# Performance work log

Measured on AMD Instinct MI355X. Metric: run time of the kernel, lower is better.

Reference implementation:

```python
import math
import jax, jax.numpy as jnp
import numpy as np

CH = 256
NUM_GROUPS = 32
EPS = 1e-5


def setup_inputs() -> dict:
    key = jax.random.key(0)
    ks = jax.random.split(key, 8)
    B, C, S = 32, CH, 32
    x = jax.random.normal(ks[0], (B, C, S, S), dtype=jnp.float32)
    t_embd = jax.random.normal(ks[1], (B, 4 * C), dtype=jnp.float32)
    gamma = jnp.ones((C,), dtype=jnp.float32)
    beta = jnp.zeros((C,), dtype=jnp.float32)
    # torch nn.Linear(ch, 3*ch): weight shape (3*ch, ch), y = x @ W.T + b
    w_attn = jax.random.normal(ks[2], (3 * C, C), dtype=jnp.float32) * (1.0 / math.sqrt(C))
    b_attn = jax.random.normal(ks[3], (3 * C,), dtype=jnp.float32) * 0.02
    w_proj = jax.random.normal(ks[4], (C, C), dtype=jnp.float32) * (1.0 / math.sqrt(C))
    b_proj = jax.random.normal(ks[5], (C,), dtype=jnp.float32) * 0.02
    return {
        "x": x, "t_embd": t_embd,
        "gamma": gamma, "beta": beta,
        "w_attn": w_attn, "b_attn": b_attn,
        "w_proj": w_proj, "b_proj": b_proj,
    }


def _group_norm(x, gamma, beta):
    # x: (B, C, S, S), normalize over (C/G, S, S) per group
    B, C, S, _ = x.shape
    xg = x.reshape(B, NUM_GROUPS, (C // NUM_GROUPS) * S * S)
    mean = jnp.mean(xg, axis=-1, keepdims=True)
    var = jnp.var(xg, axis=-1, keepdims=True)
    xn = ((xg - mean) * jax.lax.rsqrt(var + EPS)).reshape(B, C, S, S)
    return xn * gamma[None, :, None, None] + beta[None, :, None, None]


def reference(x, t_embd, gamma, beta, w_attn, b_attn, w_proj, b_proj):
    B, C, S, _ = x.shape
    norm_x = _group_norm(x, gamma, beta)
    h = jnp.transpose(norm_x, (0, 2, 3, 1))            # (B, S, S, C)
    qkv = h @ w_attn.T + b_attn                        # (B, S, S, 3C)
    q, k, v = jnp.split(qkv, 3, axis=3)
    # full spatial attention: scores over all S*S key positions
    att = jnp.einsum('bhwc,bHWc->bhwHW', q, k) * (1.0 / math.sqrt(C))
    att = jax.nn.softmax(att.reshape(B, S, S, S * S), axis=-1).reshape(B, S, S, S, S)
    o = jnp.einsum('bhwHW,bHWc->bhwc', att, v)         # (B, S, S, C)
    y = o @ w_proj.T + b_proj
    y = jnp.transpose(y, (0, 3, 1, 2))                 # (B, C, S, S)
    return x + y
```

## Files before the change

### kernel.cpp

```cpp
#include <hip/hip_runtime.h>
#include <hip/hip_bf16.h>
#include <stdint.h>
#include <stddef.h>


typedef float  f32x4  __attribute__((ext_vector_type(4)));
typedef __bf16 bf16x8 __attribute__((ext_vector_type(8)));
typedef __bf16 bf16x4 __attribute__((ext_vector_type(4)));

#define DEVI static __device__ __forceinline__

DEVI f32x4 mfma16(bf16x8 a, bf16x8 b, f32x4 c) {
  return __builtin_amdgcn_mfma_f32_16x16x32_bf16(a, b, c, 0, 0, 0);
}

DEVI f32x4 zero4() { f32x4 z = {0.f, 0.f, 0.f, 0.f}; return z; }

typedef const __attribute__((address_space(1))) void* gas_cvp;
typedef __attribute__((address_space(3))) void*       las_vp;

DEVI void gl_lds16(const __bf16* g, __bf16* l) {
  __builtin_amdgcn_global_load_lds((gas_cvp)g, (las_vp)l, 16, 0, 0);
}

#define WAIT_VM(N) asm volatile("s_waitcnt vmcnt(" #N ")" ::: "memory")
DEVI void bar() {
  asm volatile("" ::: "memory");
  __builtin_amdgcn_s_barrier();
  asm volatile("" ::: "memory");
}

__global__ __launch_bounds__(256) void cvt_weights(
    const float* __restrict__ wa, const float* __restrict__ wp,
    __bf16* __restrict__ wab, __bf16* __restrict__ wpb) {
  const int i = blockIdx.x * 256 + threadIdx.x;
  if (i < 196608) {
    wab[i] = (__bf16)wa[i];
  } else {
    const int j = i - 196608;
    if (j < 65536) wpb[j] = (__bf16)wp[j];
  }
}

__global__ __launch_bounds__(256) void gn_fused(
    const float* __restrict__ x, const float* __restrict__ gamma,
    const float* __restrict__ beta, __bf16* __restrict__ h) {
  __shared__ __align__(16) float xs[8192];
  __shared__ float redS[4], redSS[4];
  const int bg = blockIdx.x;
  const int b = bg >> 5, g = bg & 31;
  const int tid = threadIdx.x;
  const float* base = x + (size_t)bg * 8192;
  float s = 0.f, ss = 0.f;
#pragma unroll
  for (int it = 0; it < 8; ++it) {
    const int i = it * 256 + tid;
    f32x4 v = *(const f32x4*)(base + i * 4);
    *(f32x4*)(xs + i * 4) = v;
    s  += v[0] + v[1] + v[2] + v[3];
    ss += v[0]*v[0] + v[1]*v[1] + v[2]*v[2] + v[3]*v[3];
  }
#pragma unroll
  for (int m = 1; m < 64; m <<= 1) {
    s  += __shfl_xor(s,  m, 64);
    ss += __shfl_xor(ss, m, 64);
  }
  const int lane = tid & 63, wave = tid >> 6;
  if (lane == 0) { redS[wave] = s; redSS[wave] = ss; }
  __syncthreads();
  const float S  = redS[0] + redS[1] + redS[2] + redS[3];
  const float SS = redSS[0] + redSS[1] + redSS[2] + redSS[3];
  const float mu = S * (1.f / 8192.f);
  const float rstd = rsqrtf(SS * (1.f / 8192.f) - mu * mu + 1e-5f);
  float ga[8], be[8];
#pragma unroll
  for (int j = 0; j < 8; ++j) {
    const int c = g * 8 + j;
    ga[j] = gamma[c] * rstd;
    be[j] = beta[c] - mu * ga[j];
  }
  __bf16* hb = h + ((size_t)b << 18) + g * 8;
#pragma unroll
  for (int it = 0; it < 4; ++it) {
    const int p = it * 256 + tid;
    bf16x8 o8;
#pragma unroll
    for (int j = 0; j < 8; ++j)
      o8[j] = (__bf16)(xs[j * 1024 + p] * ga[j] + be[j]);
    *(bf16x8*)(hb + ((size_t)p << 8)) = o8;
  }
}

DEVI void gemm_core_k256(const __bf16* __restrict__ A0, const __bf16* __restrict__ B0,
                         __bf16* lA, __bf16* lB, int lane, int wave, f32x4 acc[4][4]) {
  const int wm = (wave >> 1) * 64;
  const int wn = (wave & 1) * 64;
  const int r15 = lane & 15, lg = lane >> 4;
#pragma unroll
  for (int i = 0; i < 4; ++i)
#pragma unroll
    for (int j = 0; j < 4; ++j) acc[i][j] = zero4();

  for (int ko = 0; ko < 4; ++ko) {
#pragma unroll
    for (int it = 0; it < 4; ++it) {
      const int q = wave * 256 + it * 64 + lane;
      const int row = q >> 3, c8 = q & 7;
      const int srcoff = row * 256 + ko * 64 + ((c8 ^ (row & 7)) << 3);
      gl_lds16(A0 + srcoff, lA + (size_t)(wave * 256 + it * 64) * 8);
      gl_lds16(B0 + srcoff, lB + (size_t)(wave * 256 + it * 64) * 8);
    }
    __syncthreads();
#pragma unroll
    for (int kk = 0; kk < 2; ++kk) {
      bf16x8 af[4], bfr[4];
#pragma unroll
      for (int i = 0; i < 4; ++i) {
        const int row = wm + i * 16 + r15;
        af[i] = *(const bf16x8*)((const char*)lA + row * 128 +
                                 (((kk * 4 + lg) ^ (row & 7)) << 4));
      }
#pragma unroll
      for (int j = 0; j < 4; ++j) {
        const int row = wn + j * 16 + r15;
        bfr[j] = *(const bf16x8*)((const char*)lB + row * 128 +
                                  (((kk * 4 + lg) ^ (row & 7)) << 4));
      }
#pragma unroll
      for (int i = 0; i < 4; ++i)
#pragma unroll
        for (int j = 0; j < 4; ++j) acc[i][j] = mfma16(af[i], bfr[j], acc[i][j]);
    }
    __syncthreads();
  }
}

__global__ __launch_bounds__(256) void qkv_gemm(
    const __bf16* __restrict__ h, const __bf16* __restrict__ wab,
    const float* __restrict__ b_attn,
    __bf16* __restrict__ q, __bf16* __restrict__ k, __bf16* __restrict__ vt) {
  __shared__ __align__(16) __bf16 lA[128 * 64], lB[128 * 64];
  const int nt = blockIdx.x, mt = blockIdx.y;
  const int tid = threadIdx.x, lane = tid & 63, wave = tid >> 6;
  f32x4 acc[4][4];
  gemm_core_k256(h + (size_t)mt * 128 * 256, wab + (size_t)nt * 128 * 256,
                 lA, lB, lane, wave, acc);

  const int wm = (wave >> 1) * 64, wn = (wave & 1) * 64;
  const int r15 = lane & 15, lg = lane >> 4;
  const int sec = nt >> 1;
  const float QS = 0.0625f * 1.44269504088896340736f;
#pragma unroll
  for (int j = 0; j < 4; ++j) {
    const int ng = nt * 128 + wn + j * 16 + r15;
    const float bias = b_attn[ng];
    const int c = ng & 255;
#pragma unroll
    for (int i = 0; i < 4; ++i) {
      const int mbase = mt * 128 + wm + i * 16 + lg * 4;
      if (sec == 0) {
#pragma unroll
        for (int r = 0; r < 4; ++r)
          q[(size_t)(mbase + r) * 256 + c] = (__bf16)((acc[i][j][r] + bias) * QS);
      } else if (sec == 1) {
#pragma unroll
        for (int r = 0; r < 4; ++r)
          k[(size_t)(mbase + r) * 256 + c] = (__bf16)(acc[i][j][r] + bias);
      } else {
        const int b = mbase >> 10, p = mbase & 1023;
        bf16x4 pk;
#pragma unroll
        for (int r = 0; r < 4; ++r) pk[r] = (__bf16)(acc[i][j][r] + bias);
        *(bf16x4*)(vt + (((size_t)(b * 256 + c)) << 10) + p) = pk;
      }
    }
  }
}

__global__ __launch_bounds__(512, 2) void attn(
    const __bf16* __restrict__ q, const __bf16* __restrict__ k,
    const __bf16* __restrict__ vt, __bf16* __restrict__ o) {
  extern __shared__ __align__(16) char smem[];

  const int bid = blockIdx.x;
  const int xcd = bid & 7, sub = bid >> 3;
  const int b = xcd * 4 + (sub & 3);
  const int qt = sub >> 2;
  const int tid = threadIdx.x, lane = tid & 63, wave = tid >> 6;
  const int r15 = lane & 15, lg = lane >> 4, rs7 = r15 & 7;
  const int m0 = qt * 128 + wave * 16;
  char* P = smem + 131072 + wave * 2048;

  const __bf16* kb = k  + ((size_t)b << 18);
  const __bf16* vb = vt + ((size_t)b << 18);

  const __bf16* qb = q + (((size_t)(b * 1024 + m0)) << 8);
  bf16x8 qf[8];
#pragma unroll
  for (int kc = 0; kc < 8; ++kc)
    qf[kc] = *(const bf16x8*)(qb + ((size_t)r15) * 256 + kc * 32 + lg * 8);

  f32x4 po[16];
#pragma unroll
  for (int d = 0; d < 16; ++d) po[d] = zero4();
  float mrun = -1e30f, lrun = 0.f;

  auto stageK = [&](int n0, int buf) {
    __bf16* dst = (__bf16*)(smem + buf * 32768);
#pragma unroll
    for (int it = 0; it < 4; ++it) {
      const int qch = it * 512 + tid;
      const int row = qch >> 5, c32 = qch & 31;
      gl_lds16(kb + (size_t)(n0 + row) * 256 + ((c32 ^ (row & 7)) << 3),
               dst + (size_t)(it * 512 + wave * 64) * 8);
    }
  };
  auto stageV = [&](int n0, int buf) {
    __bf16* dst = (__bf16*)(smem + 65536 + buf * 32768);
#pragma unroll
    for (int it = 0; it < 4; ++it) {
      const int qch = it * 512 + tid;
      const int row = qch >> 3, c8 = qch & 7;
      gl_lds16(vb + ((size_t)row << 10) + n0 + ((c8 ^ (row & 7)) << 3),
               dst + (size_t)(it * 512 + wave * 64) * 8);
    }
  };

  stageK(0, 0);
  stageV(0, 0);

  for (int kv = 0; kv < 16; ++kv) {
    const int cur = kv & 1;
    const char* lK = (const char*)smem + cur * 32768;
    const char* lV = (const char*)smem + 65536 + cur * 32768;
    if (kv < 15) {
      stageK((kv + 1) * 64, cur ^ 1);
      stageV((kv + 1) * 64, cur ^ 1);
      WAIT_VM(8);
    } else {
      WAIT_VM(0);
    }
    bar();

    f32x4 s[4];
#pragma unroll
    for (int j = 0; j < 4; ++j) s[j] = zero4();
#pragma unroll
    for (int kc = 0; kc < 8; ++kc) {
      bf16x8 kf[4];
#pragma unroll
      for (int j = 0; j < 4; ++j)
        kf[j] = *(const bf16x8*)(lK + (j * 16 + r15) * 512 +
                                 (((kc * 4 + lg) ^ rs7) << 4));
#pragma unroll
      for (int j = 0; j < 4; ++j) s[j] = mfma16(kf[j], qf[kc], s[j]);
    }
    float pmax = s[0][0];
#pragma unroll
    for (int j = 0; j < 4; ++j)
#pragma unroll
      for (int r = 0; r < 4; ++r) pmax = fmaxf(pmax, s[j][r]);
    pmax = fmaxf(pmax, __shfl_xor(pmax, 16, 64));
    pmax = fmaxf(pmax, __shfl_xor(pmax, 32, 64));
    if (!__all(pmax <= mrun + 8.f)) {
      const float mn = fmaxf(mrun, pmax);
      const float scl = exp2f(mrun - mn);
      mrun = mn;
      lrun *= scl;
#pragma unroll
      for (int d = 0; d < 16; ++d) po[d] *= scl;
    }
    float psum = 0.f;
    bf16x4 pk[4];
#pragma unroll
    for (int j = 0; j < 4; ++j)
#pragma unroll
      for (int r = 0; r < 4; ++r) {
        const float pv = exp2f(s[j][r] - mrun);
        psum += pv;
        pk[j][r] = (__bf16)pv;
      }
    psum += __shfl_xor(psum, 16, 64);
    psum += __shfl_xor(psum, 32, 64);
    lrun += psum;
#pragma unroll
    for (int j = 0; j < 4; ++j)
      *(bf16x4*)(P + r15 * 128 + ((j * 32 + lg * 8) ^ (rs7 << 4))) = pk[j];
#pragma unroll
    for (int kk = 0; kk < 2; ++kk) {
      const bf16x8 pb =
          *(const bf16x8*)(P + r15 * 128 + (((kk * 4 + lg) ^ rs7) << 4));
#pragma unroll
      for (int df = 0; df < 16; ++df) {
        const bf16x8 vf = *(const bf16x8*)(lV + (df * 16 + r15) * 128 +
                                           (((kk * 4 + lg) ^ rs7) << 4));
        po[df] = mfma16(vf, pb, po[df]);
      }
    }
    bar();
  }
  const float inv = 1.f / lrun;
  __bf16* ob = o + (((size_t)(b * 1024 + m0 + r15)) << 8);
#pragma unroll
  for (int df = 0; df < 16; ++df) {
    bf16x4 t;
#pragma unroll
    for (int r = 0; r < 4; ++r) t[r] = (__bf16)(po[df][r] * inv);
    *(bf16x4*)(ob + df * 16 + lg * 4) = t;
  }
}

__global__ __launch_bounds__(256) void proj_gemm(
    const __bf16* __restrict__ o, const __bf16* __restrict__ wpb,
    const float* __restrict__ b_proj, const float* __restrict__ x,
    float* __restrict__ out) {
  __shared__ __align__(16) __bf16 lA[128 * 64], lB[128 * 64];
  const int nt = blockIdx.x, mt = blockIdx.y;
  const int tid = threadIdx.x, lane = tid & 63, wave = tid >> 6;
  f32x4 acc[4][4];
  gemm_core_k256(o + (size_t)mt * 128 * 256, wpb + (size_t)nt * 128 * 256,
                 lA, lB, lane, wave, acc);

  const int wm = (wave >> 1) * 64, wn = (wave & 1) * 64;
  const int r15 = lane & 15, lg = lane >> 4;
#pragma unroll
  for (int j = 0; j < 4; ++j) {
    const int c = nt * 128 + wn + j * 16 + r15;
    const float bias = b_proj[c];
#pragma unroll
    for (int i = 0; i < 4; ++i) {
      const int mbase = mt * 128 + wm + i * 16 + lg * 4;
      const int b = mbase >> 10, p = mbase & 1023;
      const size_t off = (((size_t)(b * 256 + c)) << 10) + p;
      f32x4 xv = *(const f32x4*)(x + off);
      f32x4 r = acc[i][j];
      r = r + xv;
      r = r + bias;
      *(f32x4*)(out + off) = r;
    }
  }
}

extern "C" void kernel_launch(void* const* d_in, const int* in_sizes, int n_in,
                              void* d_out, int out_size, void* d_ws, size_t ws_size,
                              hipStream_t stream) {
  const float* x      = (const float*)d_in[0];
  const float* gamma  = (const float*)d_in[2];
  const float* beta   = (const float*)d_in[3];
  const float* w_attn = (const float*)d_in[4];
  const float* b_attn = (const float*)d_in[5];
  const float* w_proj = (const float*)d_in[6];
  const float* b_proj = (const float*)d_in[7];
  float* out = (float*)d_out;

  char* ws = (char*)d_ws;
  __bf16* h   = (__bf16*)(ws);
  __bf16* qb  = (__bf16*)(ws + ((size_t)16 << 20));
  __bf16* kb  = (__bf16*)(ws + ((size_t)32 << 20));
  __bf16* vtb = (__bf16*)(ws + ((size_t)48 << 20));
  __bf16* wab = (__bf16*)(ws + ((size_t)64 << 20));
  __bf16* wpb = wab + 196608;

  cvt_weights<<<1024, 256, 0, stream>>>(w_attn, w_proj, wab, wpb);
  gn_fused<<<1024, 256, 0, stream>>>(x, gamma, beta, h);
  qkv_gemm<<<dim3(6, 256), 256, 0, stream>>>(h, wab, b_attn, qb, kb, vtb);
  attn<<<256, 512, 147456, stream>>>(qb, kb, vtb, h );
  proj_gemm<<<dim3(2, 256), 256, 0, stream>>>(h, wpb, b_proj, x, out);
}
```

Baseline: 131.6 us.

## Double query rows per attention wave and load full K in GEMMs

The attention kernel now runs 4 waves per block, each handling 32 query rows as two 16-row halves. This lets every K and V fragment read from LDS feed two MFMAs, halving LDS traffic per FLOP at the cost of doubled accumulator registers. The QKV and projection GEMMs now stage the whole K=256 slice into 128KB of dynamic LDS in one pass, removing the per-k-chunk barriers. The trade-off is occupancy of one block per CU and no overlap of load with compute.

```diff
diff --git a/kernel.cpp b/kernel.cpp
--- a/kernel.cpp
+++ b/kernel.cpp
@@ -91,8 +91,8 @@
   }
 }
 
-DEVI void gemm_core_k256(const __bf16* __restrict__ A0, const __bf16* __restrict__ B0,
-                         __bf16* lA, __bf16* lB, int lane, int wave, f32x4 acc[4][4]) {
+DEVI void gemm_full(const __bf16* __restrict__ A0, const __bf16* __restrict__ B0,
+                    __bf16* lA, __bf16* lB, int lane, int wave, f32x4 acc[4][4]) {
   const int wm = (wave >> 1) * 64;
   const int wn = (wave & 1) * 64;
   const int r15 = lane & 15, lg = lane >> 4;
@@ -101,50 +101,49 @@
 #pragma unroll
     for (int j = 0; j < 4; ++j) acc[i][j] = zero4();
 
-  for (int ko = 0; ko < 4; ++ko) {
-#pragma unroll
-    for (int it = 0; it < 4; ++it) {
-      const int q = wave * 256 + it * 64 + lane;
-      const int row = q >> 3, c8 = q & 7;
-      const int srcoff = row * 256 + ko * 64 + ((c8 ^ (row & 7)) << 3);
-      gl_lds16(A0 + srcoff, lA + (size_t)(wave * 256 + it * 64) * 8);
-      gl_lds16(B0 + srcoff, lB + (size_t)(wave * 256 + it * 64) * 8);
-    }
-    __syncthreads();
-#pragma unroll
-    for (int kk = 0; kk < 2; ++kk) {
-      bf16x8 af[4], bfr[4];
-#pragma unroll
-      for (int i = 0; i < 4; ++i) {
-        const int row = wm + i * 16 + r15;
-        af[i] = *(const bf16x8*)((const char*)lA + row * 128 +
-                                 (((kk * 4 + lg) ^ (row & 7)) << 4));
-      }
-#pragma unroll
-      for (int j = 0; j < 4; ++j) {
-        const int row = wn + j * 16 + r15;
-        bfr[j] = *(const bf16x8*)((const char*)lB + row * 128 +
-                                  (((kk * 4 + lg) ^ (row & 7)) << 4));
-      }
-#pragma unroll
-      for (int i = 0; i < 4; ++i)
-#pragma unroll
-        for (int j = 0; j < 4; ++j) acc[i][j] = mfma16(af[i], bfr[j], acc[i][j]);
-    }
-    __syncthreads();
-  }
-}
-
-__global__ __launch_bounds__(256) void qkv_gemm(
+#pragma unroll
+  for (int it = 0; it < 16; ++it) {
+    const int qch = it * 256 + wave * 64 + lane;
+    const int row = qch >> 5, c32 = qch & 31;
+    const int src = row * 256 + ((c32 ^ (row & 7)) << 3);
+    gl_lds16(A0 + src, lA + (size_t)(it * 256 + wave * 64) * 8);
+    gl_lds16(B0 + src, lB + (size_t)(it * 256 + wave * 64) * 8);
+  }
+  __syncthreads();
+#pragma unroll
+  for (int kk = 0; kk < 8; ++kk) {
+    bf16x8 af[4], bfr[4];
+#pragma unroll
+    for (int i = 0; i < 4; ++i) {
+      const int row = wm + i * 16 + r15;
+      af[i] = *(const bf16x8*)((const char*)lA + row * 512 +
+                               (((kk * 4 + lg) ^ (row & 7)) << 4));
+    }
+#pragma unroll
+    for (int j = 0; j < 4; ++j) {
+      const int row = wn + j * 16 + r15;
+      bfr[j] = *(const bf16x8*)((const char*)lB + row * 512 +
+                                (((kk * 4 + lg) ^ (row & 7)) << 4));
+    }
+#pragma unroll
+    for (int i = 0; i < 4; ++i)
+#pragma unroll
+      for (int j = 0; j < 4; ++j) acc[i][j] = mfma16(af[i], bfr[j], acc[i][j]);
+  }
+}
+
+__global__ __launch_bounds__(256, 1) void qkv_gemm(
     const __bf16* __restrict__ h, const __bf16* __restrict__ wab,
     const float* __restrict__ b_attn,
     __bf16* __restrict__ q, __bf16* __restrict__ k, __bf16* __restrict__ vt) {
-  __shared__ __align__(16) __bf16 lA[128 * 64], lB[128 * 64];
+  extern __shared__ __align__(16) char gsm[];
+  __bf16* lA = (__bf16*)gsm;
+  __bf16* lB = (__bf16*)(gsm + 65536);
   const int nt = blockIdx.x, mt = blockIdx.y;
   const int tid = threadIdx.x, lane = tid & 63, wave = tid >> 6;
   f32x4 acc[4][4];
-  gemm_core_k256(h + (size_t)mt * 128 * 256, wab + (size_t)nt * 128 * 256,
-                 lA, lB, lane, wave, acc);
+  gemm_full(h + (size_t)mt * 128 * 256, wab + (size_t)nt * 128 * 256,
+            lA, lB, lane, wave, acc);
 
   const int wm = (wave >> 1) * 64, wn = (wave & 1) * 64;
   const int r15 = lane & 15, lg = lane >> 4;
@@ -177,7 +176,7 @@
   }
 }
 
-__global__ __launch_bounds__(512, 2) void attn(
+__global__ __launch_bounds__(256, 1) void attn(
     const __bf16* __restrict__ q, const __bf16* __restrict__ k,
     const __bf16* __restrict__ vt, __bf16* __restrict__ o) {
   extern __shared__ __align__(16) char smem[];
@@ -188,41 +187,45 @@
   const int qt = sub >> 2;
   const int tid = threadIdx.x, lane = tid & 63, wave = tid >> 6;
   const int r15 = lane & 15, lg = lane >> 4, rs7 = r15 & 7;
-  const int m0 = qt * 128 + wave * 16;
-  char* P = smem + 131072 + wave * 2048;
+  const int m0 = qt * 128 + wave * 32;
+  char* P = smem + 131072 + wave * 4096;
 
   const __bf16* kb = k  + ((size_t)b << 18);
   const __bf16* vb = vt + ((size_t)b << 18);
 
   const __bf16* qb = q + (((size_t)(b * 1024 + m0)) << 8);
-  bf16x8 qf[8];
-#pragma unroll
-  for (int kc = 0; kc < 8; ++kc)
-    qf[kc] = *(const bf16x8*)(qb + ((size_t)r15) * 256 + kc * 32 + lg * 8);
-
-  f32x4 po[16];
-#pragma unroll
-  for (int d = 0; d < 16; ++d) po[d] = zero4();
-  float mrun = -1e30f, lrun = 0.f;
+  bf16x8 qf[2][8];
+#pragma unroll
+  for (int qh = 0; qh < 2; ++qh)
+#pragma unroll
+    for (int kc = 0; kc < 8; ++kc)
+      qf[qh][kc] = *(const bf16x8*)(qb + (size_t)(qh * 16 + r15) * 256 + kc * 32 + lg * 8);
+
+  f32x4 po[16][2];
+#pragma unroll
+  for (int d = 0; d < 16; ++d)
+#pragma unroll
+    for (int qh = 0; qh < 2; ++qh) po[d][qh] = zero4();
+  float mrun[2] = {-1e30f, -1e30f}, lrun[2] = {0.f, 0.f};
 
   auto stageK = [&](int n0, int buf) {
     __bf16* dst = (__bf16*)(smem + buf * 32768);
 #pragma unroll
-    for (int it = 0; it < 4; ++it) {
-      const int qch = it * 512 + tid;
+    for (int it = 0; it < 8; ++it) {
+      const int qch = it * 256 + tid;
       const int row = qch >> 5, c32 = qch & 31;
       gl_lds16(kb + (size_t)(n0 + row) * 256 + ((c32 ^ (row & 7)) << 3),
-               dst + (size_t)(it * 512 + wave * 64) * 8);
+               dst + (size_t)(it * 256 + wave * 64) * 8);
     }
   };
   auto stageV = [&](int n0, int buf) {
     __bf16* dst = (__bf16*)(smem + 65536 + buf * 32768);
 #pragma unroll
-    for (int it = 0; it < 4; ++it) {
-      const int qch = it * 512 + tid;
+    for (int it = 0; it < 8; ++it) {
+      const int qch = it * 256 + tid;
       const int row = qch >> 3, c8 = qch & 7;
       gl_lds16(vb + ((size_t)row << 10) + n0 + ((c8 ^ (row & 7)) << 3),
-               dst + (size_t)(it * 512 + wave * 64) * 8);
+               dst + (size_t)(it * 256 + wave * 64) * 8);
     }
   };
 
@@ -236,15 +239,17 @@
     if (kv < 15) {
       stageK((kv + 1) * 64, cur ^ 1);
       stageV((kv + 1) * 64, cur ^ 1);
-      WAIT_VM(8);
+      WAIT_VM(16);
     } else {
       WAIT_VM(0);
     }
     bar();
 
-    f32x4 s[4];
-#pragma unroll
-    for (int j = 0; j < 4; ++j) s[j] = zero4();
+    f32x4 s[2][4];
+#pragma unroll
+    for (int qh = 0; qh < 2; ++qh)
+#pragma unroll
+      for (int j = 0; j < 4; ++j) s[qh][j] = zero4();
 #pragma unroll
     for (int kc = 0; kc < 8; ++kc) {
       bf16x8 kf[4];
@@ -253,73 +258,91 @@
         kf[j] = *(const bf16x8*)(lK + (j * 16 + r15) * 512 +
                                  (((kc * 4 + lg) ^ rs7) << 4));
 #pragma unroll
-      for (int j = 0; j < 4; ++j) s[j] = mfma16(kf[j], qf[kc], s[j]);
-    }
-    float pmax = s[0][0];
-#pragma unroll
-    for (int j = 0; j < 4; ++j)
-#pragma unroll
-      for (int r = 0; r < 4; ++r) pmax = fmaxf(pmax, s[j][r]);
-    pmax = fmaxf(pmax, __shfl_xor(pmax, 16, 64));
-    pmax = fmaxf(pmax, __shfl_xor(pmax, 32, 64));
-    if (!__all(pmax <= mrun + 8.f)) {
-      const float mn = fmaxf(mrun, pmax);
-      const float scl = exp2f(mrun - mn);
-      mrun = mn;
-      lrun *= scl;
-#pragma unroll
-      for (int d = 0; d < 16; ++d) po[d] *= scl;
-    }
-    float psum = 0.f;
-    bf16x4 pk[4];
-#pragma unroll
-    for (int j = 0; j < 4; ++j)
-#pragma unroll
-      for (int r = 0; r < 4; ++r) {
-        const float pv = exp2f(s[j][r] - mrun);
-        psum += pv;
-        pk[j][r] = (__bf16)pv;
+      for (int qh = 0; qh < 2; ++qh)
+#pragma unroll
+        for (int j = 0; j < 4; ++j) s[qh][j] = mfma16(kf[j], qf[qh][kc], s[qh][j]);
+    }
+    bf16x4 pk[2][4];
+#pragma unroll
+    for (int qh = 0; qh < 2; ++qh) {
+      float pmax = s[qh][0][0];
+#pragma unroll
+      for (int j = 0; j < 4; ++j)
+#pragma unroll
+        for (int r = 0; r < 4; ++r) pmax = fmaxf(pmax, s[qh][j][r]);
+      pmax = fmaxf(pmax, __shfl_xor(pmax, 16, 64));
+      pmax = fmaxf(pmax, __shfl_xor(pmax, 32, 64));
+      if (!__all(pmax <= mrun[qh] + 8.f)) {
+        const float mn = fmaxf(mrun[qh], pmax);
+        const float scl = exp2f(mrun[qh] - mn);
+        mrun[qh] = mn;
+        lrun[qh] *= scl;
+#pragma unroll
+        for (int d = 0; d < 16; ++d) po[d][qh] *= scl;
       }
-    psum += __shfl_xor(psum, 16, 64);
-    psum += __shfl_xor(psum, 32, 64);
-    lrun += psum;
-#pragma unroll
-    for (int j = 0; j < 4; ++j)
-      *(bf16x4*)(P + r15 * 128 + ((j * 32 + lg * 8) ^ (rs7 << 4))) = pk[j];
+      float psum = 0.f;
+#pragma unroll
+      for (int j = 0; j < 4; ++j)
+#pragma unroll
+        for (int r = 0; r < 4; ++r) {
+          const float pv = exp2f(s[qh][j][r] - mrun[qh]);
+          psum += pv;
+          pk[qh][j][r] = (__bf16)pv;
+        }
+      psum += __shfl_xor(psum, 16, 64);
+      psum += __shfl_xor(psum, 32, 64);
+      lrun[qh] += psum;
+    }
+#pragma unroll
+    for (int qh = 0; qh < 2; ++qh)
+#pragma unroll
+      for (int j = 0; j < 4; ++j)
+        *(bf16x4*)(P + (qh * 16 + r15) * 128 + ((j * 32 + lg * 8) ^ (rs7 << 4))) =
+            pk[qh][j];
 #pragma unroll
     for (int kk = 0; kk < 2; ++kk) {
-      const bf16x8 pb =
-          *(const bf16x8*)(P + r15 * 128 + (((kk * 4 + lg) ^ rs7) << 4));
+      bf16x8 pb[2];
+#pragma unroll
+      for (int qh = 0; qh < 2; ++qh)
+        pb[qh] = *(const bf16x8*)(P + (qh * 16 + r15) * 128 +
+                                  (((kk * 4 + lg) ^ rs7) << 4));
 #pragma unroll
       for (int df = 0; df < 16; ++df) {
         const bf16x8 vf = *(const bf16x8*)(lV + (df * 16 + r15) * 128 +
                                            (((kk * 4 + lg) ^ rs7) << 4));
-        po[df] = mfma16(vf, pb, po[df]);
+#pragma unroll
+        for (int qh = 0; qh < 2; ++qh) po[df][qh] = mfma16(vf, pb[qh], po[df][qh]);
       }
     }
     bar();
   }
-  const float inv = 1.f / lrun;
-  __bf16* ob = o + (((size_t)(b * 1024 + m0 + r15)) << 8);
-#pragma unroll
-  for (int df = 0; df < 16; ++df) {
-    bf16x4 t;
-#pragma unroll
-    for (int r = 0; r < 4; ++r) t[r] = (__bf16)(po[df][r] * inv);
-    *(bf16x4*)(ob + df * 16 + lg * 4) = t;
-  }
-}
-
-__global__ __launch_bounds__(256) void proj_gemm(
+  const float inv0 = 1.f / lrun[0], inv1 = 1.f / lrun[1];
+#pragma unroll
+  for (int qh = 0; qh < 2; ++qh) {
+    const float inv = qh ? inv1 : inv0;
+    __bf16* ob = o + (((size_t)(b * 1024 + m0 + qh * 16 + r15)) << 8);
+#pragma unroll
+    for (int df = 0; df < 16; ++df) {
+      bf16x4 t;
+#pragma unroll
+      for (int r = 0; r < 4; ++r) t[r] = (__bf16)(po[df][qh][r] * inv);
+      *(bf16x4*)(ob + df * 16 + lg * 4) = t;
+    }
+  }
+}
+
+__global__ __launch_bounds__(256, 1) void proj_gemm(
     const __bf16* __restrict__ o, const __bf16* __restrict__ wpb,
     const float* __restrict__ b_proj, const float* __restrict__ x,
     float* __restrict__ out) {
-  __shared__ __align__(16) __bf16 lA[128 * 64], lB[128 * 64];
+  extern __shared__ __align__(16) char gsm[];
+  __bf16* lA = (__bf16*)gsm;
+  __bf16* lB = (__bf16*)(gsm + 65536);
   const int nt = blockIdx.x, mt = blockIdx.y;
   const int tid = threadIdx.x, lane = tid & 63, wave = tid >> 6;
   f32x4 acc[4][4];
-  gemm_core_k256(o + (size_t)mt * 128 * 256, wpb + (size_t)nt * 128 * 256,
-                 lA, lB, lane, wave, acc);
+  gemm_full(o + (size_t)mt * 128 * 256, wpb + (size_t)nt * 128 * 256,
+            lA, lB, lane, wave, acc);
 
   const int wm = (wave >> 1) * 64, wn = (wave & 1) * 64;
   const int r15 = lane & 15, lg = lane >> 4;
@@ -363,7 +386,7 @@
 
   cvt_weights<<<1024, 256, 0, stream>>>(w_attn, w_proj, wab, wpb);
   gn_fused<<<1024, 256, 0, stream>>>(x, gamma, beta, h);
-  qkv_gemm<<<dim3(6, 256), 256, 0, stream>>>(h, wab, b_attn, qb, kb, vtb);
-  attn<<<256, 512, 147456, stream>>>(qb, kb, vtb, h );
-  proj_gemm<<<dim3(2, 256), 256, 0, stream>>>(h, wpb, b_proj, x, out);
-}
+  qkv_gemm<<<dim3(6, 256), 256, 131072, stream>>>(h, wab, b_attn, qb, kb, vtb);
+  attn<<<256, 256, 147456, stream>>>(qb, kb, vtb, h );
+  proj_gemm<<<dim3(2, 256), 256, 131072, stream>>>(h, wpb, b_proj, x, out);
+}
```

Result: slower. 147.8 us (+12.3%).
